# Optimization experiments

Measured on AMD Instinct MI355X. Metric: run time of the kernel, lower is better.

## Reference

```python
import jax, jax.numpy as jnp
from jax import lax
import numpy as np

# Dims matching init_kwargs / input_specs
B, R, C, CIN, COUT, W, CT = 8, 96, 64, 8, 64, 8, 4


def setup_inputs() -> dict:
    key = jax.random.key(0)
    ks = jax.random.split(key, 16)
    s = 0.05
    n = lambda k, shp: s * jax.random.normal(k, shp, jnp.float32)
    return {
        "x": jax.random.normal(ks[0], (B, R, C, CIN, 1), jnp.float32),
        "x_mark": jax.random.normal(ks[1], (B, R, C, CIN, CT), jnp.float32),
        # hidden_MLP_data: Conv1d(c_in -> c_in*c_out, k=W, groups=c_in) -> per-group in=1
        "Wd": n(ks[2], (CIN * COUT, 1, W)),
        "bd": n(ks[3], (CIN * COUT,)),
        # hidden_MLP_mark: Conv1d(c_in*CT -> c_in*c_out, k=W, groups=c_in) -> per-group in=CT
        "Wm": n(ks[4], (CIN * COUT, CT, W)),
        "bm": n(ks[5], (CIN * COUT,)),
        # gate_data: k=1 grouped conv, per-group 1 -> 2*c_out; stored einsum-friendly [g, 2*c_out]
        "Gd": n(ks[6], (CIN, 2 * COUT)),
        "bgd": n(ks[7], (CIN, 2 * COUT)),
        # gate_mark: per-group CT -> 2*c_out
        "Gm": n(ks[8], (CIN, 2 * COUT, CT)),
        "bgm": n(ks[9], (CIN, 2 * COUT)),
        # gate_hid: per-group c_out -> 2*c_out
        "Gh": n(ks[10], (CIN, 2 * COUT, COUT)),
        "bgh": n(ks[11], (CIN, 2 * COUT)),
        # fc: Conv1d(c_in*c_out -> c_in*c_out, k=seq_R, groups=c_in) -> [g, o, i, R]
        "Fw": n(ks[12], (CIN, COUT, COUT, R)),
        "bf": n(ks[13], (CIN, COUT)),
    }


def _grouped_conv1d(xa, w, b, groups):
    # xa: [N, Cin, L], w: [Cout, Cin//groups, K]
    y = lax.conv_general_dilated(
        xa, w, window_strides=(1,), padding="VALID",
        dimension_numbers=("NCH", "OIH", "NCH"), feature_group_count=groups)
    return y + b[None, :, None]


def reference(x, x_mark, Wd, bd, Wm, bm, Gd, bgd, Gm, bgm, Gh, bgh, Fw, bf):
    Bv, Rv, Cv, cin, _ = x.shape
    ct = x_mark.shape[-1]
    cout = Gh.shape[-1]
    Wk = Wd.shape[-1]

    # ---- deal(): causal windowed grouped conv over R ----
    # pad W zeros in front along R, drop last step -> length R+W-1, VALID conv k=W -> R
    xz = jnp.concatenate([jnp.zeros((Bv, Wk, Cv, cin, 1), x.dtype), x], axis=1)
    xa = xz.transpose(0, 2, 3, 4, 1).reshape(Bv * Cv, cin, Rv + Wk)[:, :, :-1]
    Hd = _grouped_conv1d(xa, Wd, bd, cin)  # [B*C, cin*cout, R]

    mz = jnp.concatenate([jnp.zeros((Bv, Wk, Cv, cin, ct), x.dtype), x_mark], axis=1)
    ma = mz.transpose(0, 2, 3, 4, 1).reshape(Bv * Cv, cin * ct, Rv + Wk)[:, :, :-1]
    Hm = _grouped_conv1d(ma, Wm, bm, cin)

    hid = (Hd + Hm).reshape(Bv, Cv, cin, cout, Rv).transpose(0, 4, 1, 2, 3)  # [B,R,C,cin,cout]

    # ---- gated_unit(): kernel-1 grouped convs == per-group matmuls ----
    xs = x[..., 0]  # [B,R,C,cin]
    g = jnp.einsum("brcg,go->brcgo", xs, Gd) + bgd
    g = g + jnp.einsum("brcgt,got->brcgo", x_mark, Gm) + bgm
    g = g + jnp.einsum("brcgi,goi->brcgo", hid, Gh) + bgh
    sg = jax.nn.sigmoid(g[..., :cout])
    tg = jnp.tanh(g[..., cout:])
    hid = hid * sg + (1.0 - sg) * tg  # [B,R,C,cin,cout]

    # ---- fc: grouped conv with kernel==R -> full contraction over (in-chan, R) ----
    out = jnp.einsum("brcgi,goir->bcgo", hid, Fw) + bf  # [B,C,cin,cout]
    return out
```

## Files before the change

kernel.cpp:

```cpp
#include <hip/hip_runtime.h>
#include <hip/hip_bf16.h>
#include <math.h>

namespace {

typedef __attribute__((ext_vector_type(8))) short bh8;
typedef __attribute__((ext_vector_type(4))) short sh4;
typedef __attribute__((ext_vector_type(4))) float fx4;

constexpr int Rn = 96, Cn = 64, CINn = 8, COUTn = 64;
constexpr int NPOS = 8 * 96 * 64 * 8;
constexpr int PPG  = 8 * 96 * 64;
constexpr float NLOG2E = -1.4426950408889634f;
constexpr float LOG2E2 =  2.8853900817779268f;
constexpr size_t FEAT_OFF = 0;
constexpr size_t FWT_OFF  = (size_t)NPOS * 16;
constexpr size_t CA_OFF   = FWT_OFF + (size_t)NPOS * 16;
constexpr size_t GWT_OFF  = CA_OFF + 65536;
constexpr size_t PART_OFF = GWT_OFF + 196608;

__device__ inline ushort f2b(float f) {
  __hip_bfloat16 h = __float2bfloat16(f);
  return __builtin_bit_cast(ushort, h);
}
__device__ inline int swz8(int bc, int rr, int ib) {
  return (bc * 1024 + rr * 128 + ib) ^ (((rr + bc) & 7) << 4);
}
__device__ inline int fswz(int l, int bc) {
  return (l * 16 + (bc ^ (l & 7))) * 8;
}

#define MFMA16(a, b, c) __builtin_amdgcn_mfma_f32_16x16x32_bf16((a), (b), (c), 0, 0, 0)

__global__ __launch_bounds__(512)
void prep_k(const float* __restrict__ x, const float* __restrict__ xm,
            const float* __restrict__ Fw, const float* __restrict__ Gh,
            const float* __restrict__ Gd, const float* __restrict__ bgd,
            const float* __restrict__ Gm, const float* __restrict__ bgm,
            const float* __restrict__ bgh,
            const float* __restrict__ Wd, const float* __restrict__ bd,
            const float* __restrict__ Wm, const float* __restrict__ bm,
            ushort* __restrict__ feat, ushort* __restrict__ FwT,
            ushort* __restrict__ GWT, ushort* __restrict__ cA)
{
  __shared__ float tile[64 * 97];
  const int bid = blockIdx.x, t = threadIdx.x;
  if (bid < 768) {
    const int pos = bid * 512 + t;
    const float xs = x[pos];
    const fx4 m = *(const fx4*)(xm + (size_t)pos * 4);
    bh8 o;
    o[0] = (short)f2b(xs);
    o[1] = (short)f2b(m[0]); o[2] = (short)f2b(m[1]);
    o[3] = (short)f2b(m[2]); o[4] = (short)f2b(m[3]);
    o[5] = (short)0x3F80; o[6] = 0; o[7] = 0;
    const int g = pos & 7, pb = pos >> 3;
    *(bh8*)(feat + ((size_t)g * PPG + pb) * 8) = o;
  } else if (bid < 1280) {
    const int go = bid - 768;
    const float* src = Fw + (size_t)go * 6144;
    ushort* dst = FwT + (size_t)go * 6144;
#pragma unroll
    for (int it = 0; it < 12; ++it) {
      const int idx = t + it * 512;
      tile[(idx / 96) * 97 + (idx % 96)] = src[idx];
    }
    __syncthreads();
#pragma unroll
    for (int it = 0; it < 12; ++it) {
      const int idx = t + it * 512;
      const int r = idx >> 6, i = idx & 63;
      dst[idx] = f2b(tile[i * 97 + r]);
    }
  } else if (bid < 1344) {
    const int e = (bid - 1280) * 512 + t;
    const int j = e & 7, lp = (e >> 3) & 63, sub = (e >> 9) & 7, g = e >> 12;
    const int il = lp >> 4, mr = lp & 15;
    const int o2 = (sub >> 2) * 64 + (sub & 3) * 16 + mr;
    float v = 0.f;
    if (il == 0) {
      if (j == 0)      v = Gd[g * 128 + o2];
      else if (j <= 4) v = Gm[(size_t)(g * 128 + o2) * 4 + (j - 1)];
      else if (j == 5) v = bgd[g * 128 + o2] + bgm[g * 128 + o2] + bgh[g * 128 + o2];
    }
    v *= (sub >= 4) ? LOG2E2 : NLOG2E;
    GWT[((size_t)(g * 24 + sub * 3 + 2) * 64 + lp) * 8 + j] = f2b(v);
  } else if (bid < 1408) {
    const int e = (bid - 1344) * 512 + t;
    const int g = e >> 12, co = (e >> 6) & 63, k = e & 63;
    const int tap = k >> 3, tch = k & 7;
    float v = 0.f;
    if (tch == 0)      v = Wd[(g * 64 + co) * 8 + tap];
    else if (tch <= 4) v = Wm[((g * 64 + co) * 4 + (tch - 1)) * 8 + tap];
    else if (tch == 5 && tap == 0) v = bd[g * 64 + co] + bm[g * 64 + co];
    cA[e] = f2b(v);
  } else {
    const int e = (bid - 1408) * 512 + t;
    const int row = e >> 6, k = e & 63;
    const int g = row >> 7, o2 = row & 127;
    const int tap = k >> 3, tch = k & 7;
    const float* pA; int sA = 0; float mA = 0.f, mB = 0.f;
    const float* pB;
    if (tch == 0)      { pA = Wd + (size_t)(g * 64) * 8 + tap; sA = 8;  mA = 1.f; }
    else if (tch <= 4) { pA = Wm + ((size_t)(g * 64) * 4 + (tch - 1)) * 8 + tap; sA = 32; mA = 1.f; }
    else if (tch == 5 && tap == 0) { pA = bd + g * 64; sA = 1; mA = 1.f; mB = 1.f; }
    else               { pA = Wd; }
    pB = (mB != 0.f) ? (bm + g * 64) : pA;
    const float* gh = Gh + (size_t)(g * 128 + o2) * 64;
    float acc = 0.f;
#pragma unroll 8
    for (int i = 0; i < 64; ++i) {
      const float wv = fmaf(mB, pB[i], mA * pA[i * sA]);
      acc = fmaf(gh[i], wv, acc);
    }
    acc *= (o2 >= 64) ? LOG2E2 : NLOG2E;
    const int half = o2 >> 6, s = (o2 >> 4) & 3, mr = o2 & 15;
    const int sub = half * 4 + s, fs = k >> 5, lp = ((k & 31) >> 3) * 16 + mr, j = k & 7;
    GWT[((size_t)(g * 24 + sub * 3 + fs) * 64 + lp) * 8 + j] = f2b(acc);
  }
}

__global__ __launch_bounds__(512, 2)
void fused_v11(const ushort* __restrict__ feat, const ushort* __restrict__ FwT,
               const ushort* __restrict__ cA, const ushort* __restrict__ GWT,
               float* __restrict__ part)
{
  __shared__ __align__(16) ushort sTab[16384];
  __shared__ __align__(16) char sGat[2][16384];
  __shared__ __align__(16) ushort sFeat[2][2048];
  __shared__ float sRed[1024];

  const int t    = threadIdx.x;
  const int lane = t & 63;
  const int w    = t >> 6;
  const int il   = lane >> 4;
  const int mr   = lane & 15;
  const int bid  = blockIdx.x;
  const int g    = bid & 7;
  const int bcT  = (bid >> 3) & 31;
  const int chh  = bid >> 8;
  const ushort* fg = feat + (size_t)g * PPG * 8;
  const int s4   = w & 3, hf = w >> 2;
  const int tb   = lane * 8;

  const int pglob = w * 16 + mr;
  const int cbcl = pglob >> 3, crr = pglob & 7;

  const int sl = t >> 4, sbc = t & 15;
  const int sbcg = bcT * 16 + sbc;
  const size_t sprow = (size_t)((sbcg >> 6) * 96) * 64 + (sbcg & 63);
  const int sadr = fswz(sl, sbc);
  const bh8 zpad = {0, 0, 0, 0, 0, (short)0x3F80, 0, 0};

  *(bh8*)&sTab[w * 512 + tb] =
      *(const bh8*)(cA + g * 4096 + ((w >> 1) * 16 + mr) * 64 + (w & 1) * 32 + il * 8);
  {
    const ushort* gsrc = GWT + (size_t)g * 12288;
#pragma unroll
    for (int it = 0; it < 3; ++it) {
      const int idx = it * 512 + t;
      *(bh8*)&sTab[4096 + idx * 8] = *(const bh8*)(gsrc + idx * 8);
    }
  }
  if (t < 256) {
    const int q = chh * 48 - 8 + sl;
    *(bh8*)&sFeat[0][sadr] =
        (q >= 0) ? *(const bh8*)(fg + (sprow + (size_t)q * 64) * 8) : zpad;
  }

  const int a_b0 = fswz(crr + il, cbcl);
  const int a_b1 = fswz(crr + il + 4, cbcl);
  const int a_bx = fswz(crr + 8, cbcl);
  int wadr[4];
#pragma unroll
  for (int s = 0; s < 4; ++s) wadr[s] = swz8(cbcl, crr, s * 32 + il * 8);
  const ushort* fb0 = FwT + ((size_t)(g * 64 + s4 * 16 + mr) * 96) * 64 + 32 * hf + 8 * il;

  fx4 facc = {0.f, 0.f, 0.f, 0.f};
  __syncthreads();

  int cur = 0;
#pragma unroll 1
  for (int k6 = 0; k6 < 6; ++k6) {
    const int r0 = chh * 48 + k6 * 8;

    bh8 stg;
    const bool do_stage = (t < 256) && (k6 < 5);
    if (do_stage)
      stg = *(const bh8*)(fg + (sprow + (size_t)(r0 + sl) * 64) * 8);
    bh8 aF[8];
    {
      const ushort* fb = fb0 + (size_t)r0 * 64;
#pragma unroll
      for (int f = 0; f < 8; ++f) aF[f] = *(const bh8*)(fb + f * 64);
    }

    const bh8 b0 = *(const bh8*)&sFeat[cur][a_b0];
    const bh8 b1 = *(const bh8*)&sFeat[cur][a_b1];
    const bh8 bx = *(const bh8*)&sFeat[cur][a_bx];

    fx4 ah[4];
#pragma unroll
    for (int s = 0; s < 4; ++s) {
      const bh8 a0 = *(const bh8*)&sTab[(s * 2 + 0) * 512 + tb];
      const bh8 a1 = *(const bh8*)&sTab[(s * 2 + 1) * 512 + tb];
      fx4 a = {0.f, 0.f, 0.f, 0.f};
      a = MFMA16(a0, b0, a);
      a = MFMA16(a1, b1, a);
      ah[s] = a;
    }

    char* gbuf = sGat[k6 & 1];
#pragma unroll
    for (int s = 0; s < 4; ++s) {
      const int bs = (8 + s * 3) * 512 + tb;
      const int bt = (8 + (4 + s) * 3) * 512 + tb;
      fx4 aS = {0.f,0.f,0.f,0.f}, aT = {0.f,0.f,0.f,0.f};
      aS = MFMA16(*(const bh8*)&sTab[bs],        b0, aS);
      aS = MFMA16(*(const bh8*)&sTab[bs + 512],  b1, aS);
      aS = MFMA16(*(const bh8*)&sTab[bs + 1024], bx, aS);
      aT = MFMA16(*(const bh8*)&sTab[bt],        b0, aT);
      aT = MFMA16(*(const bh8*)&sTab[bt + 512],  b1, aT);
      aT = MFMA16(*(const bh8*)&sTab[bt + 1024], bx, aT);
      sh4 o4;
#pragma unroll
      for (int cc = 0; cc < 4; ++cc) {
        const float sig = __builtin_amdgcn_rcpf(1.f + exp2f(aS[cc]));
        const float y   = exp2f(aT[cc]);
        const float th  = (y - 1.f) * __builtin_amdgcn_rcpf(y + 1.f);
        o4[cc] = (short)f2b(fmaf(sig, ah[s][cc] - th, th));
      }
      *(sh4*)(gbuf + wadr[s]) = o4;
    }

    if (do_stage) *(bh8*)&sFeat[cur ^ 1][sadr] = stg;
    __syncthreads();

#pragma unroll
    for (int f = 0; f < 8; ++f) {
      const bh8 bF = *(const bh8*)(gbuf + swz8(mr, f, 64 * hf + 16 * il));
      facc = MFMA16(aF[f], bF, facc);
    }
    cur ^= 1;
  }

  if (hf == 1) {
#pragma unroll
    for (int cc = 0; cc < 4; ++cc)
      sRed[s4 * 256 + (4 * il + cc) * 16 + mr] = facc[cc];
  }
  __syncthreads();
  if (hf == 0) {
    float* pp = part + ((size_t)(chh * 8 + g) * 32 + bcT) * 1024;
#pragma unroll
    for (int cc = 0; cc < 4; ++cc)
      pp[mr * 64 + s4 * 16 + 4 * il + cc] = facc[cc] + sRed[s4 * 256 + (4 * il + cc) * 16 + mr];
  }
}

__global__ __launch_bounds__(256)
void reduce_k(const float* __restrict__ part, const float* __restrict__ bf,
              float* __restrict__ out)
{
  const int e = blockIdx.x * 256 + threadIdx.x;
  const int o = e & 63, g = (e >> 6) & 7, bcg = e >> 9;
  const int bcT = bcg >> 4, bcl = bcg & 15;
  const float s = bf[g * 64 + o]
      + part[((size_t)(0 * 8 + g) * 32 + bcT) * 1024 + bcl * 64 + o]
      + part[((size_t)(1 * 8 + g) * 32 + bcT) * 1024 + bcl * 64 + o];
  out[e] = s;
}

}

extern "C" void kernel_launch(void* const* d_in, const int* in_sizes, int n_in,
                              void* d_out, int out_size, void* d_ws, size_t ws_size,
                              hipStream_t stream) {
  const float* x   = (const float*)d_in[0];
  const float* xm  = (const float*)d_in[1];
  const float* Wd  = (const float*)d_in[2];
  const float* bd  = (const float*)d_in[3];
  const float* Wm  = (const float*)d_in[4];
  const float* bm  = (const float*)d_in[5];
  const float* Gd  = (const float*)d_in[6];
  const float* bgd = (const float*)d_in[7];
  const float* Gm  = (const float*)d_in[8];
  const float* bgm = (const float*)d_in[9];
  const float* Gh  = (const float*)d_in[10];
  const float* bgh = (const float*)d_in[11];
  const float* Fw  = (const float*)d_in[12];
  const float* bf  = (const float*)d_in[13];
  float* outp = (float*)d_out;

  ushort* feat = (ushort*)((char*)d_ws + FEAT_OFF);
  ushort* FwT  = (ushort*)((char*)d_ws + FWT_OFF);
  ushort* cA   = (ushort*)((char*)d_ws + CA_OFF);
  ushort* GWT  = (ushort*)((char*)d_ws + GWT_OFF);
  float*  part = (float*)((char*)d_ws + PART_OFF);

  prep_k<<<dim3(1536), dim3(512), 0, stream>>>(
      x, xm, Fw, Gh, Gd, bgd, Gm, bgm, bgh, Wd, bd, Wm, bm, feat, FwT, GWT, cA);
  fused_v11<<<dim3(512), dim3(512), 0, stream>>>(feat, FwT, cA, GWT, part);
  reduce_k<<<dim3(1024), dim3(256), 0, stream>>>(part, bf, outp);
}
```

Measured before the change: 56.03 us.

## Fuse feature packing and split-R reduction into single 1024-thread main kernel

```diff
diff --git a/kernel.cpp b/kernel.cpp
--- a/kernel.cpp
+++ b/kernel.cpp
@@ -8,56 +8,40 @@
 typedef __attribute__((ext_vector_type(4))) short sh4;
 typedef __attribute__((ext_vector_type(4))) float fx4;
 
-constexpr int Rn = 96, Cn = 64, CINn = 8, COUTn = 64;
-constexpr int NPOS = 8 * 96 * 64 * 8;
 constexpr int PPG  = 8 * 96 * 64;
 constexpr float NLOG2E = -1.4426950408889634f;
 constexpr float LOG2E2 =  2.8853900817779268f;
-constexpr size_t FEAT_OFF = 0;
-constexpr size_t FWT_OFF  = (size_t)NPOS * 16;
-constexpr size_t CA_OFF   = FWT_OFF + (size_t)NPOS * 16;
-constexpr size_t GWT_OFF  = CA_OFF + 65536;
-constexpr size_t PART_OFF = GWT_OFF + 196608;
+constexpr size_t FWT_OFF = 0;
+constexpr size_t CA_OFF  = 6291456;
+constexpr size_t GWT_OFF = CA_OFF + 65536;
 
 __device__ inline ushort f2b(float f) {
   __hip_bfloat16 h = __float2bfloat16(f);
   return __builtin_bit_cast(ushort, h);
 }
-__device__ inline int swz8(int bc, int rr, int ib) {
-  return (bc * 1024 + rr * 128 + ib) ^ (((rr + bc) & 7) << 4);
+__device__ inline int swzG(int bc, int rr, int ib) {
+  return (bc * 2048 + rr * 128 + ib) ^ (((rr + bc) & 7) << 4);
 }
 __device__ inline int fswz(int l, int bc) {
-  return (l * 16 + (bc ^ (l & 7))) * 8;
+  return (l * 16 + ((bc + l) & 15)) * 8;
 }
 
 #define MFMA16(a, b, c) __builtin_amdgcn_mfma_f32_16x16x32_bf16((a), (b), (c), 0, 0, 0)
 
 __global__ __launch_bounds__(512)
-void prep_k(const float* __restrict__ x, const float* __restrict__ xm,
-            const float* __restrict__ Fw, const float* __restrict__ Gh,
+void prep_k(const float* __restrict__ Fw, const float* __restrict__ Gh,
             const float* __restrict__ Gd, const float* __restrict__ bgd,
             const float* __restrict__ Gm, const float* __restrict__ bgm,
             const float* __restrict__ bgh,
             const float* __restrict__ Wd, const float* __restrict__ bd,
             const float* __restrict__ Wm, const float* __restrict__ bm,
-            ushort* __restrict__ feat, ushort* __restrict__ FwT,
-            ushort* __restrict__ GWT, ushort* __restrict__ cA)
+            ushort* __restrict__ FwT, ushort* __restrict__ GWT,
+            ushort* __restrict__ cA)
 {
   __shared__ float tile[64 * 97];
   const int bid = blockIdx.x, t = threadIdx.x;
-  if (bid < 768) {
-    const int pos = bid * 512 + t;
-    const float xs = x[pos];
-    const fx4 m = *(const fx4*)(xm + (size_t)pos * 4);
-    bh8 o;
-    o[0] = (short)f2b(xs);
-    o[1] = (short)f2b(m[0]); o[2] = (short)f2b(m[1]);
-    o[3] = (short)f2b(m[2]); o[4] = (short)f2b(m[3]);
-    o[5] = (short)0x3F80; o[6] = 0; o[7] = 0;
-    const int g = pos & 7, pb = pos >> 3;
-    *(bh8*)(feat + ((size_t)g * PPG + pb) * 8) = o;
-  } else if (bid < 1280) {
-    const int go = bid - 768;
+  if (bid < 512) {
+    const int go = bid;
     const float* src = Fw + (size_t)go * 6144;
     ushort* dst = FwT + (size_t)go * 6144;
 #pragma unroll
@@ -72,8 +56,8 @@
       const int r = idx >> 6, i = idx & 63;
       dst[idx] = f2b(tile[i * 97 + r]);
     }
-  } else if (bid < 1344) {
-    const int e = (bid - 1280) * 512 + t;
+  } else if (bid < 576) {
+    const int e = (bid - 512) * 512 + t;
     const int j = e & 7, lp = (e >> 3) & 63, sub = (e >> 9) & 7, g = e >> 12;
     const int il = lp >> 4, mr = lp & 15;
     const int o2 = (sub >> 2) * 64 + (sub & 3) * 16 + mr;
@@ -85,8 +69,8 @@
     }
     v *= (sub >= 4) ? LOG2E2 : NLOG2E;
     GWT[((size_t)(g * 24 + sub * 3 + 2) * 64 + lp) * 8 + j] = f2b(v);
-  } else if (bid < 1408) {
-    const int e = (bid - 1344) * 512 + t;
+  } else if (bid < 640) {
+    const int e = (bid - 576) * 512 + t;
     const int g = e >> 12, co = (e >> 6) & 63, k = e & 63;
     const int tap = k >> 3, tch = k & 7;
     float v = 0.f;
@@ -95,7 +79,7 @@
     else if (tch == 5 && tap == 0) v = bd[g * 64 + co] + bm[g * 64 + co];
     cA[e] = f2b(v);
   } else {
-    const int e = (bid - 1408) * 512 + t;
+    const int e = (bid - 640) * 512 + t;
     const int row = e >> 6, k = e & 63;
     const int g = row >> 7, o2 = row & 127;
     const int tap = k >> 3, tch = k & 7;
@@ -120,15 +104,16 @@
   }
 }
 
-__global__ __launch_bounds__(512, 2)
-void fused_v11(const ushort* __restrict__ feat, const ushort* __restrict__ FwT,
-               const ushort* __restrict__ cA, const ushort* __restrict__ GWT,
-               float* __restrict__ part)
+__global__ __launch_bounds__(1024, 1)
+void fused_v12(const float* __restrict__ x, const float* __restrict__ xm,
+               const ushort* __restrict__ FwT, const ushort* __restrict__ cA,
+               const ushort* __restrict__ GWT, const float* __restrict__ bf,
+               float* __restrict__ out)
 {
   __shared__ __align__(16) ushort sTab[16384];
-  __shared__ __align__(16) char sGat[2][16384];
-  __shared__ __align__(16) ushort sFeat[2][2048];
-  __shared__ float sRed[1024];
+  __shared__ __align__(16) char  sGat[2][32768];
+  __shared__ __align__(16) ushort sFeat[2][3072];
+  __shared__ float sRed[4096];
 
   const int t    = threadIdx.x;
   const int lane = t & 63;
@@ -137,44 +122,53 @@
   const int mr   = lane & 15;
   const int bid  = blockIdx.x;
   const int g    = bid & 7;
-  const int bcT  = (bid >> 3) & 31;
-  const int chh  = bid >> 8;
-  const ushort* fg = feat + (size_t)g * PPG * 8;
-  const int s4   = w & 3, hf = w >> 2;
+  const int bcT  = bid >> 3;
+  const int s4   = w & 3, hq = w >> 2;
   const int tb   = lane * 8;
-
-  const int pglob = w * 16 + mr;
-  const int cbcl = pglob >> 3, crr = pglob & 7;
 
   const int sl = t >> 4, sbc = t & 15;
   const int sbcg = bcT * 16 + sbc;
-  const size_t sprow = (size_t)((sbcg >> 6) * 96) * 64 + (sbcg & 63);
+  const size_t sposb = ((size_t)(sbcg >> 6) * 96) * 64 + (sbcg & 63);
   const int sadr = fswz(sl, sbc);
-  const bh8 zpad = {0, 0, 0, 0, 0, (short)0x3F80, 0, 0};
-
-  *(bh8*)&sTab[w * 512 + tb] =
-      *(const bh8*)(cA + g * 4096 + ((w >> 1) * 16 + mr) * 64 + (w & 1) * 32 + il * 8);
+
+  if (w < 8)
+    *(bh8*)&sTab[w * 512 + tb] =
+        *(const bh8*)(cA + g * 4096 + ((w >> 1) * 16 + mr) * 64 + (w & 1) * 32 + il * 8);
   {
     const ushort* gsrc = GWT + (size_t)g * 12288;
 #pragma unroll
-    for (int it = 0; it < 3; ++it) {
-      const int idx = it * 512 + t;
-      *(bh8*)&sTab[4096 + idx * 8] = *(const bh8*)(gsrc + idx * 8);
-    }
-  }
-  if (t < 256) {
-    const int q = chh * 48 - 8 + sl;
-    *(bh8*)&sFeat[0][sadr] =
-        (q >= 0) ? *(const bh8*)(fg + (sprow + (size_t)q * 64) * 8) : zpad;
-  }
-
-  const int a_b0 = fswz(crr + il, cbcl);
-  const int a_b1 = fswz(crr + il + 4, cbcl);
-  const int a_bx = fswz(crr + 8, cbcl);
+    for (int it = 0; it < 2; ++it) {
+      const int idx = it * 1024 + t;
+      if (idx < 1536)
+        *(bh8*)&sTab[4096 + idx * 8] = *(const bh8*)(gsrc + idx * 8);
+    }
+  }
+  if (t < 384) {
+    const int q = sl - 8;
+    bh8 o;
+    if (q >= 0) {
+      const size_t pi = (sposb + (size_t)q * 64) * 8 + g;
+      const float xs = x[pi];
+      const fx4 m = *(const fx4*)(xm + pi * 4);
+      o[0] = (short)f2b(xs);
+      o[1] = (short)f2b(m[0]); o[2] = (short)f2b(m[1]);
+      o[3] = (short)f2b(m[2]); o[4] = (short)f2b(m[3]);
+      o[5] = (short)0x3F80; o[6] = 0; o[7] = 0;
+    } else {
+      bh8 z = {0, 0, 0, 0, 0, (short)0x3F80, 0, 0};
+      o = z;
+    }
+    *(bh8*)&sFeat[0][sadr] = o;
+  }
+
+  const int a_b0 = fswz(mr + il, w);
+  const int a_b1 = fswz(mr + il + 4, w);
+  const int a_bx = fswz(mr + 8, w);
   int wadr[4];
 #pragma unroll
-  for (int s = 0; s < 4; ++s) wadr[s] = swz8(cbcl, crr, s * 32 + il * 8);
-  const ushort* fb0 = FwT + ((size_t)(g * 64 + s4 * 16 + mr) * 96) * 64 + 32 * hf + 8 * il;
+  for (int s = 0; s < 4; ++s) wadr[s] = swzG(w, mr, s * 32 + il * 8);
+  const ushort* fb0 = FwT + ((size_t)(g * 64 + s4 * 16 + mr) * 96) * 64 + hq * 16 + (il & 1) * 8;
+  const int rsub = il >> 1;
 
   fx4 facc = {0.f, 0.f, 0.f, 0.f};
   __syncthreads();
@@ -182,18 +176,23 @@
   int cur = 0;
 #pragma unroll 1
   for (int k6 = 0; k6 < 6; ++k6) {
-    const int r0 = chh * 48 + k6 * 8;
+    const int r0 = k6 * 16;
 
     bh8 stg;
-    const bool do_stage = (t < 256) && (k6 < 5);
-    if (do_stage)
-      stg = *(const bh8*)(fg + (sprow + (size_t)(r0 + sl) * 64) * 8);
+    const bool do_stage = (t < 384) && (k6 < 5);
+    if (do_stage) {
+      const size_t pi = (sposb + (size_t)(r0 + 8 + sl) * 64) * 8 + g;
+      const float xs = x[pi];
+      const fx4 m = *(const fx4*)(xm + pi * 4);
+      stg[0] = (short)f2b(xs);
+      stg[1] = (short)f2b(m[0]); stg[2] = (short)f2b(m[1]);
+      stg[3] = (short)f2b(m[2]); stg[4] = (short)f2b(m[3]);
+      stg[5] = (short)0x3F80; stg[6] = 0; stg[7] = 0;
+    }
     bh8 aF[8];
-    {
-      const ushort* fb = fb0 + (size_t)r0 * 64;
-#pragma unroll
-      for (int f = 0; f < 8; ++f) aF[f] = *(const bh8*)(fb + f * 64);
-    }
+#pragma unroll
+    for (int f = 0; f < 8; ++f)
+      aF[f] = *(const bh8*)(fb0 + (size_t)(r0 + f * 2 + rsub) * 64);
 
     const bh8 b0 = *(const bh8*)&sFeat[cur][a_b0];
     const bh8 b1 = *(const bh8*)&sFeat[cur][a_b1];
@@ -210,7 +209,7 @@
       ah[s] = a;
     }
 
-    char* gbuf = sGat[k6 & 1];
+    char* gbuf = sGat[cur];
 #pragma unroll
     for (int s = 0; s < 4; ++s) {
       const int bs = (8 + s * 3) * 512 + tb;
@@ -227,7 +226,7 @@
       for (int cc = 0; cc < 4; ++cc) {
         const float sig = __builtin_amdgcn_rcpf(1.f + exp2f(aS[cc]));
         const float y   = exp2f(aT[cc]);
-        const float th  = (y - 1.f) * __builtin_amdgcn_rcpf(y + 1.f);
+        const float th  = fmaf(-2.f, __builtin_amdgcn_rcpf(y + 1.f), 1.f);
         o4[cc] = (short)f2b(fmaf(sig, ah[s][cc] - th, th));
       }
       *(sh4*)(gbuf + wadr[s]) = o4;
@@ -238,37 +237,25 @@
 
 #pragma unroll
     for (int f = 0; f < 8; ++f) {
-      const bh8 bF = *(const bh8*)(gbuf + swz8(mr, f, 64 * hf + 16 * il));
+      const bh8 bF = *(const bh8*)(gbuf + swzG(mr, f * 2 + rsub, hq * 32 + (il & 1) * 16));
       facc = MFMA16(aF[f], bF, facc);
     }
     cur ^= 1;
   }
 
-  if (hf == 1) {
-#pragma unroll
-    for (int cc = 0; cc < 4; ++cc)
-      sRed[s4 * 256 + (4 * il + cc) * 16 + mr] = facc[cc];
-  }
+#pragma unroll
+  for (int cc = 0; cc < 4; ++cc)
+    sRed[(hq * 4 + s4) * 256 + (4 * il + cc) * 16 + mr] = facc[cc];
   __syncthreads();
-  if (hf == 0) {
-    float* pp = part + ((size_t)(chh * 8 + g) * 32 + bcT) * 1024;
-#pragma unroll
-    for (int cc = 0; cc < 4; ++cc)
-      pp[mr * 64 + s4 * 16 + 4 * il + cc] = facc[cc] + sRed[s4 * 256 + (4 * il + cc) * 16 + mr];
-  }
-}
-
-__global__ __launch_bounds__(256)
-void reduce_k(const float* __restrict__ part, const float* __restrict__ bf,
-              float* __restrict__ out)
-{
-  const int e = blockIdx.x * 256 + threadIdx.x;
-  const int o = e & 63, g = (e >> 6) & 7, bcg = e >> 9;
-  const int bcT = bcg >> 4, bcl = bcg & 15;
-  const float s = bf[g * 64 + o]
-      + part[((size_t)(0 * 8 + g) * 32 + bcT) * 1024 + bcl * 64 + o]
-      + part[((size_t)(1 * 8 + g) * 32 + bcT) * 1024 + bcl * 64 + o];
-  out[e] = s;
+  {
+    const int o = t & 63, bc = t >> 6;
+    const int os4 = o >> 4, ol = o & 15;
+    float s = bf[g * 64 + o];
+#pragma unroll
+    for (int hh = 0; hh < 4; ++hh)
+      s += sRed[(hh * 4 + os4) * 256 + ol * 16 + bc];
+    out[((size_t)(bcT * 16 + bc) * 8 + g) * 64 + o] = s;
+  }
 }
 
 }
@@ -292,14 +279,11 @@
   const float* bf  = (const float*)d_in[13];
   float* outp = (float*)d_out;
 
-  ushort* feat = (ushort*)((char*)d_ws + FEAT_OFF);
-  ushort* FwT  = (ushort*)((char*)d_ws + FWT_OFF);
-  ushort* cA   = (ushort*)((char*)d_ws + CA_OFF);
-  ushort* GWT  = (ushort*)((char*)d_ws + GWT_OFF);
-  float*  part = (float*)((char*)d_ws + PART_OFF);
-
-  prep_k<<<dim3(1536), dim3(512), 0, stream>>>(
-      x, xm, Fw, Gh, Gd, bgd, Gm, bgm, bgh, Wd, bd, Wm, bm, feat, FwT, GWT, cA);
-  fused_v11<<<dim3(512), dim3(512), 0, stream>>>(feat, FwT, cA, GWT, part);
-  reduce_k<<<dim3(1024), dim3(256), 0, stream>>>(part, bf, outp);
-}
+  ushort* FwT = (ushort*)((char*)d_ws + FWT_OFF);
+  ushort* cA  = (ushort*)((char*)d_ws + CA_OFF);
+  ushort* GWT = (ushort*)((char*)d_ws + GWT_OFF);
+
+  prep_k<<<dim3(768), dim3(512), 0, stream>>>(
+      Fw, Gh, Gd, bgd, Gm, bgm, bgh, Wd, bd, Wm, bm, FwT, GWT, cA);
+  fused_v12<<<dim3(256), dim3(1024), 0, stream>>>(x, xm, FwT, cA, GWT, bf, outp);
+}
```

After: 60.51 us. 8.0% more time.
